# Kernel tuning notes

Measured on AMD Instinct MI355X. Metric: run time of the kernel, lower is better.

Reference implementation:

```python
import jax, jax.numpy as jnp
import numpy as np

ATT = 16          # attention_size -> window = 2*ATT+1 = 33
HID = 512         # middle hidden size


def setup_inputs() -> dict:
    key = jax.random.key(0)
    ks = jax.random.split(key, 7)
    B, S, D_IN = 4, 2048, 256
    def xav(k, shape):
        fan_in, fan_out = shape[0], shape[1]
        std = np.sqrt(2.0 / (fan_in + fan_out))
        return jax.random.normal(k, shape, dtype=jnp.float32) * std
    return {
        "x": jax.random.normal(ks[0], (B, S, D_IN), dtype=jnp.float32),
        "Wq": xav(ks[1], (HID, HID)),
        "Wk": xav(ks[2], (HID, HID)),
        "Wv": xav(ks[3], (HID, HID)),
        "W0": xav(ks[4], (D_IN, HID)),
        "b0": jnp.zeros((1, 1, HID), dtype=jnp.float32),
        "W1": xav(ks[5], (HID, HID)),
        "b1": jnp.zeros((1, 1, HID), dtype=jnp.float32),
        "Wout": xav(ks[6], (HID, 2)),
        "bout": jnp.zeros((1, 1, 2), dtype=jnp.float32),
    }


def _local_windows(h, A):
    # h: [B, S, H] -> nei: [B, S, 2A+1, H], nei[b,t,j] = h[b, t+A-j] (zero padded)
    S = h.shape[1]
    padded = jnp.pad(h, ((0, 0), (A, A), (0, 0)))
    t = jnp.arange(S)[:, None]
    j = jnp.arange(2 * A + 1)[None, :]
    idx = t + 2 * A - j  # padded index of h[t + A - j]
    return padded[:, idx, :]


def reference(x, Wq, Wk, Wv, W0, b0, W1, b1, Wout, bout):
    scale = jnp.float32(np.sqrt(float(HID)))
    # pre-attention MLP layer(s)
    h = jax.nn.relu(x @ W0 + b0)                       # [B,S,H]
    nei = _local_windows(h, ATT)                       # [B,S,W,H]
    q = h @ Wq                                         # [B,S,H]
    k = nei @ Wk                                       # [B,S,W,H]
    v = nei @ Wv                                       # [B,S,W,H]
    dist = jnp.einsum('bsd,bswd->bsw', q, k) / scale   # [B,S,W]
    attn = jax.nn.softmax(dist, axis=-1)               # [B,S,W]
    ctx = jnp.einsum('bsw,bswd->bsd', attn, v)         # [B,S,H]
    # post-attention MLP layers
    h2 = jax.nn.relu(ctx @ W1 + b1)
    out = h2 @ Wout + bout                             # [B,S,2]
    return out, attn[:, :, None, :]  # attn shape [B,S,1,W] as in torch
```

## Files before the change

kernel.cpp:

```cpp
#include <hip/hip_runtime.h>

#define S_LEN 2048
#define HID 512
#define DIN 256
#define WIN 33
#define MROWS 8192
#define VTB 2080
#define VTROW 8320
#define SCALE_INV 0.04419417382415922f

typedef __attribute__((ext_vector_type(8))) short short8;
typedef __attribute__((ext_vector_type(4))) float f32x4;

__device__ __forceinline__ unsigned short f2bf(float f) {
    unsigned u = __builtin_bit_cast(unsigned, f);
    u += 0x7fffu + ((u >> 16) & 1u);
    return (unsigned short)(u >> 16);
}
__device__ __forceinline__ float bf2f(unsigned short h) {
    unsigned u = ((unsigned)h) << 16;
    return __builtin_bit_cast(float, u);
}
__device__ __forceinline__ void gl_lds16(const unsigned short* g, unsigned short* l) {
    __builtin_amdgcn_global_load_lds(
        (__attribute__((address_space(1))) unsigned int*)(g),
        (__attribute__((address_space(3))) unsigned int*)(l),
        16, 0, 0);
}

__global__ __launch_bounds__(256) void prep_kernel(
    const float* __restrict__ x,
    const float* __restrict__ Wq, const float* __restrict__ Wk,
    const float* __restrict__ Wv, const float* __restrict__ W0,
    const float* __restrict__ W1, const float* __restrict__ bout,
    unsigned short* __restrict__ xb, unsigned short* __restrict__ Wt0,
    unsigned short* __restrict__ Wtqkv, unsigned short* __restrict__ Wt1,
    unsigned short* __restrict__ Vt, float* __restrict__ outp)
{
    __shared__ float tile[32][33];
    const int blk = blockIdx.x, tid = threadIdx.x;
    if (blk < 2048) {
        int i = (blk * 256 + tid) * 4;
        float4 v = *(const float4*)(x + i);
        unsigned lo = (unsigned)f2bf(v.x) | ((unsigned)f2bf(v.y) << 16);
        unsigned hi = (unsigned)f2bf(v.z) | ((unsigned)f2bf(v.w) << 16);
        uint2 p; p.x = lo; p.y = hi;
        *(uint2*)(xb + i) = p;
    } else if (blk < 2064) {
        int i = ((blk - 2048) * 256 + tid) * 4;
        float4 o; o.x = bout[0]; o.y = bout[1]; o.z = bout[0]; o.w = bout[1];
        *(float4*)(outp + i) = o;
    } else if (blk < 2320) {
        int t = (blk - 2064) * 256 + tid;
        int v = t >> 7, s = t & 127;
        int b = s >> 5, p = s & 31;
        int off = (p < 16) ? p : (2048 + p);
        Vt[(size_t)v * VTROW + b * VTB + off] = 0;
    } else {
        int tt = blk - 2320;
        const float* in; unsigned short* out; int K, kt, nt;
        if (tt < 128) { in = W0; out = Wt0; K = DIN; kt = tt & 7; nt = tt >> 3; }
        else {
            int z = (tt - 128) >> 8, r = (tt - 128) & 255;
            kt = r & 15; nt = r >> 4; K = HID;
            if (z == 0)      { in = Wq; out = Wtqkv; }
            else if (z == 1) { in = Wk; out = Wtqkv + 512 * 512; }
            else if (z == 2) { in = Wv; out = Wtqkv + 2 * 512 * 512; }
            else             { in = W1; out = Wt1; }
        }
        int k0 = kt * 32, n0 = nt * 32;
        int tx = tid & 31, ty = tid >> 5;
        for (int j = 0; j < 32; j += 8)
            tile[ty + j][tx] = in[(size_t)(k0 + ty + j) * HID + n0 + tx];
        __syncthreads();
        for (int j = 0; j < 32; j += 8)
            out[(size_t)(n0 + ty + j) * K + k0 + tx] = f2bf(tile[tx][ty + j]);
    }
}

template<int K, int MODE>
__global__ __launch_bounds__(256) void gemm128_kernel(
    const unsigned short* __restrict__ A,
    const unsigned short* __restrict__ Bt,
    const float* __restrict__ bias,
    unsigned short* __restrict__ C0,
    unsigned short* __restrict__ C1,
    unsigned short* __restrict__ C2,
    const float* __restrict__ Wout,
    float* __restrict__ outp)
{
    __shared__ __align__(16) unsigned short SMEM[16384];
    const int tid = threadIdx.x;
    const int lane = tid & 63, wid = tid >> 6;
    const int bn = blockIdx.x, bm = blockIdx.y;
    const int wr = wid >> 1, wc = wid & 1;
    const int r16 = lane & 15, kq = lane >> 4;
    const int NT = K / 32;

    f32x4 acc[4][4] = {};

    const int c0 = tid, c1 = tid + 256;
    const unsigned short* aS0 = A + (size_t)(bm * 128 + (c0 & 127)) * K + (c0 >> 7) * 8;
    const unsigned short* aS1 = A + (size_t)(bm * 128 + (c1 & 127)) * K + (c1 >> 7) * 8;
    const unsigned short* bS0 = Bt + (size_t)(bn * 128 + (c0 & 127)) * K + (c0 >> 7) * 8;
    const unsigned short* bS1 = Bt + (size_t)(bn * 128 + (c1 & 127)) * K + (c1 >> 7) * 8;

    #define STAGE(buf, kt) do { \
        gl_lds16(aS0 + (kt) * 32, SMEM + (buf) * 8192 + c0 * 8); \
        gl_lds16(aS1 + (kt) * 32, SMEM + (buf) * 8192 + c1 * 8); \
        gl_lds16(bS0 + (kt) * 32, SMEM + (buf) * 8192 + 4096 + c0 * 8); \
        gl_lds16(bS1 + (kt) * 32, SMEM + (buf) * 8192 + 4096 + c1 * 8); \
    } while (0)

    STAGE(0, 0);
    for (int kt = 0; kt < NT; ++kt) {
        const int cur = kt & 1;
        if (kt + 1 < NT) {
            STAGE(cur ^ 1, kt + 1);
            asm volatile("s_waitcnt vmcnt(4)" ::: "memory");
        } else {
            asm volatile("s_waitcnt vmcnt(0)" ::: "memory");
        }
        __builtin_amdgcn_sched_barrier(0);
        __builtin_amdgcn_s_barrier();
        __builtin_amdgcn_sched_barrier(0);

        const unsigned short* ab = SMEM + cur * 8192;
        const unsigned short* bb = ab + 4096;
        short8 af[4], bfr[4];
        #pragma unroll
        for (int mi = 0; mi < 4; ++mi)
            af[mi] = *(const short8*)(ab + kq * 1024 + (wr * 64 + mi * 16 + r16) * 8);
        #pragma unroll
        for (int ni = 0; ni < 4; ++ni)
            bfr[ni] = *(const short8*)(bb + kq * 1024 + (wc * 64 + ni * 16 + r16) * 8);
        #pragma unroll
        for (int mi = 0; mi < 4; ++mi)
            #pragma unroll
            for (int ni = 0; ni < 4; ++ni)
                acc[mi][ni] = __builtin_amdgcn_mfma_f32_16x16x32_bf16(af[mi], bfr[ni], acc[mi][ni], 0, 0, 0);

        asm volatile("s_waitcnt lgkmcnt(0)" ::: "memory");
        __builtin_amdgcn_sched_barrier(0);
        __builtin_amdgcn_s_barrier();
        __builtin_amdgcn_sched_barrier(0);
    }
    #undef STAGE

    if constexpr (MODE == 0) {
        #pragma unroll
        for (int mi = 0; mi < 4; ++mi) {
            int row0 = bm * 128 + wr * 64 + mi * 16 + kq * 4;
            #pragma unroll
            for (int ni = 0; ni < 4; ++ni) {
                int col = bn * 128 + wc * 64 + ni * 16 + r16;
                float bv = bias[col];
                #pragma unroll
                for (int r = 0; r < 4; ++r) {
                    float v = fmaxf(acc[mi][ni][r] + bv, 0.0f);
                    C0[(size_t)(row0 + r) * HID + col] = f2bf(v);
                }
            }
        }
    } else if constexpr (MODE == 1) {
        if (bn < 8) {
            unsigned short* dst = (bn < 4) ? C0 : C1;
            int cb = (bn & 3) * 128 + wc * 64;
            #pragma unroll
            for (int mi = 0; mi < 4; ++mi) {
                int row0 = bm * 128 + wr * 64 + mi * 16 + kq * 4;
                #pragma unroll
                for (int ni = 0; ni < 4; ++ni) {
                    int col = cb + ni * 16 + r16;
                    #pragma unroll
                    for (int r = 0; r < 4; ++r)
                        dst[(size_t)(row0 + r) * HID + col] = f2bf(acc[mi][ni][r]);
                }
            }
        } else {
            const int bb  = (bm * 128) >> 11;
            const int tl0 = (bm * 128) & 2047;
            #pragma unroll
            for (int p = 0; p < 2; ++p) {
                if (wc == p) {
                    #pragma unroll
                    for (int mi = 0; mi < 4; ++mi) {
                        int ttw = wr * 64 + mi * 16 + kq * 4;
                        #pragma unroll
                        for (int ni = 0; ni < 4; ++ni) {
                            int vv = ni * 16 + r16;
                            unsigned lo = (unsigned)f2bf(acc[mi][ni][0]) | ((unsigned)f2bf(acc[mi][ni][1]) << 16);
                            unsigned hi = (unsigned)f2bf(acc[mi][ni][2]) | ((unsigned)f2bf(acc[mi][ni][3]) << 16);
                            uint2 pk; pk.x = lo; pk.y = hi;
                            *(uint2*)&SMEM[vv * 128 + (ttw ^ ((vv & 7) << 3))] = pk;
                        }
                    }
                }
                __syncthreads();
                #pragma unroll
                for (int it = 0; it < 4; ++it) {
                    int vv  = (tid >> 4) + it * 16;
                    int tt8 = (tid & 15) * 8;
                    uint4 q = *(const uint4*)&SMEM[vv * 128 + (tt8 ^ ((vv & 7) << 3))];
                    int vg = (bn - 8) * 128 + p * 64 + vv;
                    *(uint4*)(C2 + (size_t)vg * VTROW + bb * VTB + 16 + tl0 + tt8) = q;
                }
                __syncthreads();
            }
        }
    } else {
        float o0[16], o1[16];
        #pragma unroll
        for (int t2 = 0; t2 < 16; ++t2) { o0[t2] = 0.0f; o1[t2] = 0.0f; }
        #pragma unroll
        for (int ni = 0; ni < 4; ++ni) {
            int col = bn * 128 + wc * 64 + ni * 16 + r16;
            float bv = bias[col];
            float2 wv = *(const float2*)(Wout + col * 2);
            #pragma unroll
            for (int mi = 0; mi < 4; ++mi)
                #pragma unroll
                for (int r = 0; r < 4; ++r) {
                    float v = fmaxf(acc[mi][ni][r] + bv, 0.0f);
                    o0[mi * 4 + r] += v * wv.x;
                    o1[mi * 4 + r] += v * wv.y;
                }
        }
        #pragma unroll
        for (int s = 1; s < 16; s <<= 1)
            #pragma unroll
            for (int t2 = 0; t2 < 16; ++t2) {
                o0[t2] += __shfl_xor(o0[t2], s);
                o1[t2] += __shfl_xor(o1[t2], s);
            }
        if (r16 == 0) {
            #pragma unroll
            for (int mi = 0; mi < 4; ++mi)
                #pragma unroll
                for (int r = 0; r < 4; ++r) {
                    int row = bm * 128 + wr * 64 + mi * 16 + kq * 4 + r;
                    atomicAdd(&outp[(size_t)row * 2],     o0[mi * 4 + r]);
                    atomicAdd(&outp[(size_t)row * 2 + 1], o1[mi * 4 + r]);
                }
        }
    }
}

__global__ __launch_bounds__(256) void attn_kernel(
    const unsigned short* __restrict__ Qb,
    const unsigned short* __restrict__ Kb,
    const unsigned short* __restrict__ Vt,
    float* __restrict__ attn_out,
    unsigned short* __restrict__ ctx)
{
    __shared__ __align__(16) float Sl[4][32][66];
    __shared__ __align__(16) unsigned short Pl[32 * 64];
    const int tid = threadIdx.x;
    const int lane = tid & 63;
    const int w = tid >> 6;
    const int t0g = blockIdx.x * 32;
    const int b = t0g >> 11;
    const int t0 = t0g & 2047;
    const int r16 = lane & 15, kq = lane >> 4;

    f32x4 s[2][4] = {};
    const unsigned short* qbase = Qb + (size_t)t0g * HID + w * 128 + kq * 8;
    const unsigned short* kbase = Kb + (long)(t0g - 16) * HID + w * 128 + kq * 8;
    #pragma unroll
    for (int ks = 0; ks < 4; ++ks) {
        short8 a0 = *(const short8*)(qbase + (size_t)r16 * HID + ks * 32);
        short8 a1 = *(const short8*)(qbase + (size_t)(16 + r16) * HID + ks * 32);
        #pragma unroll
        for (int ni = 0; ni < 4; ++ni) {
            short8 bf = *(const short8*)(kbase + (size_t)(ni * 16 + r16) * HID + ks * 32);
            s[0][ni] = __builtin_amdgcn_mfma_f32_16x16x32_bf16(a0, bf, s[0][ni], 0, 0, 0);
            s[1][ni] = __builtin_amdgcn_mfma_f32_16x16x32_bf16(a1, bf, s[1][ni], 0, 0, 0);
        }
    }
    #pragma unroll
    for (int mi = 0; mi < 2; ++mi)
        #pragma unroll
        for (int ni = 0; ni < 4; ++ni)
            #pragma unroll
            for (int r = 0; r < 4; ++r)
                Sl[w][mi * 16 + kq * 4 + r][ni * 16 + r16] = s[mi][ni][r];
    __syncthreads();

    {
        const int i = tid >> 3;
        const int c8 = (tid & 7) * 8;
        float sv[8];
        #pragma unroll
        for (int cc = 0; cc < 8; ++cc) {
            float a = Sl[0][i][c8 + cc] + Sl[1][i][c8 + cc]
                    + Sl[2][i][c8 + cc] + Sl[3][i][c8 + cc];
            int m = c8 + cc;
            bool inb = (m >= i) && (m <= i + 32);
            int krow = t0 + m - 16;
            bool inseq = (krow >= 0) && (krow < S_LEN);
            sv[cc] = inb ? (inseq ? a * SCALE_INV : 0.0f) : -INFINITY;
        }
        float mx = sv[0];
        #pragma unroll
        for (int cc = 1; cc < 8; ++cc) mx = fmaxf(mx, sv[cc]);
        mx = fmaxf(mx, __shfl_xor(mx, 1));
        mx = fmaxf(mx, __shfl_xor(mx, 2));
        mx = fmaxf(mx, __shfl_xor(mx, 4));
        float es = 0.0f;
        #pragma unroll
        for (int cc = 0; cc < 8; ++cc) { sv[cc] = __expf(sv[cc] - mx); es += sv[cc]; }
        es += __shfl_xor(es, 1);
        es += __shfl_xor(es, 2);
        es += __shfl_xor(es, 4);
        float inv = 1.0f / es;
        unsigned short pb[8];
        #pragma unroll
        for (int cc = 0; cc < 8; ++cc) {
            float p = sv[cc] * inv;
            pb[cc] = f2bf(p);
            int m = c8 + cc;
            if (m >= i && m <= i + 32)
                attn_out[(size_t)(t0g + i) * WIN + (i + 32 - m)] = p;
        }
        uint4 pk;
        pk.x = (unsigned)pb[0] | ((unsigned)pb[1] << 16);
        pk.y = (unsigned)pb[2] | ((unsigned)pb[3] << 16);
        pk.z = (unsigned)pb[4] | ((unsigned)pb[5] << 16);
        pk.w = (unsigned)pb[6] | ((unsigned)pb[7] << 16);
        *(uint4*)((char*)Pl + i * 128 + ((c8 * 2) ^ ((i & 7) << 4))) = pk;
    }
    __syncthreads();

    f32x4 c[2][8] = {};
    const char* plb = (const char*)Pl;
    const unsigned short* vtb = Vt + (size_t)b * VTB + t0;
    #pragma unroll
    for (int ks = 0; ks < 2; ++ks) {
        int cb = ks * 64 + kq * 16;
        short8 a0 = *(const short8*)(plb + r16 * 128 + (cb ^ ((r16 & 7) << 4)));
        short8 a1 = *(const short8*)(plb + (16 + r16) * 128 + (cb ^ ((r16 & 7) << 4)));
        #pragma unroll
        for (int nd = 0; nd < 8; ++nd) {
            const unsigned short* vp = vtb + (size_t)(w * 128 + nd * 16 + r16) * VTROW + ks * 32 + kq * 8;
            short8 bf = *(const short8*)vp;
            c[0][nd] = __builtin_amdgcn_mfma_f32_16x16x32_bf16(a0, bf, c[0][nd], 0, 0, 0);
            c[1][nd] = __builtin_amdgcn_mfma_f32_16x16x32_bf16(a1, bf, c[1][nd], 0, 0, 0);
        }
    }
    #pragma unroll
    for (int mi = 0; mi < 2; ++mi) {
        int row0 = t0g + mi * 16 + kq * 4;
        #pragma unroll
        for (int nd = 0; nd < 8; ++nd) {
            int col = w * 128 + nd * 16 + r16;
            #pragma unroll
            for (int r = 0; r < 4; ++r)
                ctx[(size_t)(row0 + r) * HID + col] = f2bf(c[mi][nd][r]);
        }
    }
}

extern "C" void kernel_launch(void* const* d_in, const int* in_sizes, int n_in,
                              void* d_out, int out_size, void* d_ws, size_t ws_size,
                              hipStream_t stream)
{
    const float* x    = (const float*)d_in[0];
    const float* Wq   = (const float*)d_in[1];
    const float* Wk   = (const float*)d_in[2];
    const float* Wv   = (const float*)d_in[3];
    const float* W0   = (const float*)d_in[4];
    const float* b0   = (const float*)d_in[5];
    const float* W1   = (const float*)d_in[6];
    const float* b1   = (const float*)d_in[7];
    const float* Wout = (const float*)d_in[8];
    const float* bout = (const float*)d_in[9];

    char* ws = (char*)d_ws;
    unsigned short* xb    = (unsigned short*)(ws + 0);
    unsigned short* Wt0   = (unsigned short*)(ws + (4u  << 20));
    unsigned short* Wtqkv = (unsigned short*)(ws + 4456448u);
    unsigned short* Wt1   = (unsigned short*)(ws + 6029312u);
    unsigned short* hB    = (unsigned short*)(ws + (8u  << 20));
    unsigned short* Qb    = (unsigned short*)(ws + (16u << 20));
    unsigned short* Kb    = (unsigned short*)(ws + (24u << 20));
    unsigned short* Vt    = (unsigned short*)(ws + (32u << 20));
    unsigned short* ctxB  = (unsigned short*)(ws + (41u << 20));

    float* outp  = (float*)d_out;
    float* attnp = (float*)d_out + MROWS * 2;

    prep_kernel<<<3472, 256, 0, stream>>>(x, Wq, Wk, Wv, W0, W1, bout,
                                          xb, Wt0, Wtqkv, Wt1, Vt, outp);

    gemm128_kernel<DIN, 0><<<dim3(4, 64), 256, 0, stream>>>(
        xb, Wt0, b0, hB, nullptr, nullptr, nullptr, nullptr);

    gemm128_kernel<HID, 1><<<dim3(12, 64), 256, 0, stream>>>(
        hB, Wtqkv, nullptr, Qb, Kb, Vt, nullptr, nullptr);

    attn_kernel<<<256, 256, 0, stream>>>(Qb, Kb, Vt, attnp, ctxB);

    gemm128_kernel<HID, 2><<<dim3(4, 64), 256, 0, stream>>>(
        ctxB, Wt1, b1, nullptr, nullptr, nullptr, Wout, outp);
}
```

Baseline: 147.8 us.

## Fuse post-attention MLP and output projection into the attention kernel

The attention kernel now keeps the context tile in LDS and runs the ctx@W1 GEMM, ReLU and Wout projection itself, writing final outputs directly with bout added. This removes the separate GEMM launch, the ctx round-trip through global memory, and the atomicAdd reduction. In exchange each of only 256 blocks does a 32x512x512 GEMM reading W1 from global/L2 without LDS staging, which may lower parallelism and raise LDS use per block.

New measurement: 151.1 us. +2.2%, slower.

```diff
diff --git a/kernel.cpp b/kernel.cpp
--- a/kernel.cpp
+++ b/kernel.cpp
@@ -85,9 +85,7 @@
     const float* __restrict__ bias,
     unsigned short* __restrict__ C0,
     unsigned short* __restrict__ C1,
-    unsigned short* __restrict__ C2,
-    const float* __restrict__ Wout,
-    float* __restrict__ outp)
+    unsigned short* __restrict__ C2)
 {
     __shared__ __align__(16) unsigned short SMEM[16384];
     const int tid = threadIdx.x;
@@ -162,7 +160,7 @@
                 }
             }
         }
-    } else if constexpr (MODE == 1) {
+    } else {
         if (bn < 8) {
             unsigned short* dst = (bn < 4) ? C0 : C1;
             int cb = (bn & 3) * 128 + wc * 64;
@@ -208,41 +206,6 @@
                 __syncthreads();
             }
         }
-    } else {
-        float o0[16], o1[16];
-        #pragma unroll
-        for (int t2 = 0; t2 < 16; ++t2) { o0[t2] = 0.0f; o1[t2] = 0.0f; }
-        #pragma unroll
-        for (int ni = 0; ni < 4; ++ni) {
-            int col = bn * 128 + wc * 64 + ni * 16 + r16;
-            float bv = bias[col];
-            float2 wv = *(const float2*)(Wout + col * 2);
-            #pragma unroll
-            for (int mi = 0; mi < 4; ++mi)
-                #pragma unroll
-                for (int r = 0; r < 4; ++r) {
-                    float v = fmaxf(acc[mi][ni][r] + bv, 0.0f);
-                    o0[mi * 4 + r] += v * wv.x;
-                    o1[mi * 4 + r] += v * wv.y;
-                }
-        }
-        #pragma unroll
-        for (int s = 1; s < 16; s <<= 1)
-            #pragma unroll
-            for (int t2 = 0; t2 < 16; ++t2) {
-                o0[t2] += __shfl_xor(o0[t2], s);
-                o1[t2] += __shfl_xor(o1[t2], s);
-            }
-        if (r16 == 0) {
-            #pragma unroll
-            for (int mi = 0; mi < 4; ++mi)
-                #pragma unroll
-                for (int r = 0; r < 4; ++r) {
-                    int row = bm * 128 + wr * 64 + mi * 16 + kq * 4 + r;
-                    atomicAdd(&outp[(size_t)row * 2],     o0[mi * 4 + r]);
-                    atomicAdd(&outp[(size_t)row * 2 + 1], o1[mi * 4 + r]);
-                }
-        }
     }
 }
 
@@ -250,11 +213,17 @@
     const unsigned short* __restrict__ Qb,
     const unsigned short* __restrict__ Kb,
     const unsigned short* __restrict__ Vt,
+    const unsigned short* __restrict__ W1t,
+    const float* __restrict__ b1,
+    const float* __restrict__ Wout,
+    const float* __restrict__ bout,
     float* __restrict__ attn_out,
-    unsigned short* __restrict__ ctx)
+    float* __restrict__ outp)
 {
     __shared__ __align__(16) float Sl[4][32][66];
     __shared__ __align__(16) unsigned short Pl[32 * 64];
+    __shared__ __align__(16) unsigned short Cl[32 * 512];
+    __shared__ float Ol[4][32][2];
     const int tid = threadIdx.x;
     const int lane = tid & 63;
     const int w = tid >> 6;
@@ -332,31 +301,95 @@
     __syncthreads();
 
     f32x4 c[2][8] = {};
-    const char* plb = (const char*)Pl;
-    const unsigned short* vtb = Vt + (size_t)b * VTB + t0;
+    {
+        const char* plb = (const char*)Pl;
+        const unsigned short* vtb = Vt + (size_t)b * VTB + t0;
+        #pragma unroll
+        for (int ks = 0; ks < 2; ++ks) {
+            int cb = ks * 64 + kq * 16;
+            short8 a0 = *(const short8*)(plb + r16 * 128 + (cb ^ ((r16 & 7) << 4)));
+            short8 a1 = *(const short8*)(plb + (16 + r16) * 128 + (cb ^ ((r16 & 7) << 4)));
+            #pragma unroll
+            for (int nd = 0; nd < 8; ++nd) {
+                const unsigned short* vp = vtb + (size_t)(w * 128 + nd * 16 + r16) * VTROW + ks * 32 + kq * 8;
+                short8 bf = *(const short8*)vp;
+                c[0][nd] = __builtin_amdgcn_mfma_f32_16x16x32_bf16(a0, bf, c[0][nd], 0, 0, 0);
+                c[1][nd] = __builtin_amdgcn_mfma_f32_16x16x32_bf16(a1, bf, c[1][nd], 0, 0, 0);
+            }
+        }
+    }
+
     #pragma unroll
-    for (int ks = 0; ks < 2; ++ks) {
-        int cb = ks * 64 + kq * 16;
-        short8 a0 = *(const short8*)(plb + r16 * 128 + (cb ^ ((r16 & 7) << 4)));
-        short8 a1 = *(const short8*)(plb + (16 + r16) * 128 + (cb ^ ((r16 & 7) << 4)));
-        #pragma unroll
-        for (int nd = 0; nd < 8; ++nd) {
-            const unsigned short* vp = vtb + (size_t)(w * 128 + nd * 16 + r16) * VTROW + ks * 32 + kq * 8;
-            short8 bf = *(const short8*)vp;
-            c[0][nd] = __builtin_amdgcn_mfma_f32_16x16x32_bf16(a0, bf, c[0][nd], 0, 0, 0);
-            c[1][nd] = __builtin_amdgcn_mfma_f32_16x16x32_bf16(a1, bf, c[1][nd], 0, 0, 0);
-        }
-    }
-    #pragma unroll
-    for (int mi = 0; mi < 2; ++mi) {
-        int row0 = t0g + mi * 16 + kq * 4;
-        #pragma unroll
-        for (int nd = 0; nd < 8; ++nd) {
-            int col = w * 128 + nd * 16 + r16;
-            #pragma unroll
-            for (int r = 0; r < 4; ++r)
-                ctx[(size_t)(row0 + r) * HID + col] = f2bf(c[mi][nd][r]);
-        }
+    for (int mi = 0; mi < 2; ++mi)
+        #pragma unroll
+        for (int nd = 0; nd < 8; ++nd)
+            #pragma unroll
+            for (int r = 0; r < 4; ++r) {
+                int row = mi * 16 + kq * 4 + r;
+                int byte = row * 1024 + (w * 128 + nd * 16 + r16) * 2;
+                *(unsigned short*)((char*)Cl + (byte ^ ((row & 7) << 4))) = f2bf(c[mi][nd][r]);
+            }
+    __syncthreads();
+
+    f32x4 g[2][8] = {};
+    {
+        const char* clb = (const char*)Cl;
+        const unsigned short* w1b = W1t + (size_t)(w * 128) * HID + kq * 8;
+        #pragma unroll 4
+        for (int ks = 0; ks < 16; ++ks) {
+            int r0 = r16, r1 = 16 + r16;
+            short8 af0 = *(const short8*)(clb + ((r0 * 1024 + ks * 64 + kq * 16) ^ ((r0 & 7) << 4)));
+            short8 af1 = *(const short8*)(clb + ((r1 * 1024 + ks * 64 + kq * 16) ^ ((r1 & 7) << 4)));
+            #pragma unroll
+            for (int ni = 0; ni < 8; ++ni) {
+                short8 bf = *(const short8*)(w1b + (size_t)(ni * 16 + r16) * HID + ks * 32);
+                g[0][ni] = __builtin_amdgcn_mfma_f32_16x16x32_bf16(af0, bf, g[0][ni], 0, 0, 0);
+                g[1][ni] = __builtin_amdgcn_mfma_f32_16x16x32_bf16(af1, bf, g[1][ni], 0, 0, 0);
+            }
+        }
+    }
+
+    {
+        float o0[8], o1[8];
+        #pragma unroll
+        for (int t2 = 0; t2 < 8; ++t2) { o0[t2] = 0.0f; o1[t2] = 0.0f; }
+        #pragma unroll
+        for (int ni = 0; ni < 8; ++ni) {
+            int col = w * 128 + ni * 16 + r16;
+            float bv = b1[col];
+            float2 wv = *(const float2*)(Wout + col * 2);
+            #pragma unroll
+            for (int mi = 0; mi < 2; ++mi)
+                #pragma unroll
+                for (int r = 0; r < 4; ++r) {
+                    float v = fmaxf(g[mi][ni][r] + bv, 0.0f);
+                    o0[mi * 4 + r] += v * wv.x;
+                    o1[mi * 4 + r] += v * wv.y;
+                }
+        }
+        #pragma unroll
+        for (int s2 = 1; s2 < 16; s2 <<= 1)
+            #pragma unroll
+            for (int t2 = 0; t2 < 8; ++t2) {
+                o0[t2] += __shfl_xor(o0[t2], s2);
+                o1[t2] += __shfl_xor(o1[t2], s2);
+            }
+        if (r16 == 0) {
+            #pragma unroll
+            for (int mi = 0; mi < 2; ++mi)
+                #pragma unroll
+                for (int r = 0; r < 4; ++r) {
+                    int row = mi * 16 + kq * 4 + r;
+                    Ol[w][row][0] = o0[mi * 4 + r];
+                    Ol[w][row][1] = o1[mi * 4 + r];
+                }
+        }
+    }
+    __syncthreads();
+    if (tid < 64) {
+        int row = tid >> 1, cc = tid & 1;
+        float sum = Ol[0][row][cc] + Ol[1][row][cc] + Ol[2][row][cc] + Ol[3][row][cc] + bout[cc];
+        outp[(size_t)(t0g + row) * 2 + cc] = sum;
     }
 }
 
@@ -384,7 +417,6 @@
     unsigned short* Qb    = (unsigned short*)(ws + (16u << 20));
     unsigned short* Kb    = (unsigned short*)(ws + (24u << 20));
     unsigned short* Vt    = (unsigned short*)(ws + (32u << 20));
-    unsigned short* ctxB  = (unsigned short*)(ws + (41u << 20));
 
     float* outp  = (float*)d_out;
     float* attnp = (float*)d_out + MROWS * 2;
@@ -393,13 +425,11 @@
                                           xb, Wt0, Wtqkv, Wt1, Vt, outp);
 
     gemm128_kernel<DIN, 0><<<dim3(4, 64), 256, 0, stream>>>(
-        xb, Wt0, b0, hB, nullptr, nullptr, nullptr, nullptr);
+        xb, Wt0, b0, hB, nullptr, nullptr);
 
     gemm128_kernel<HID, 1><<<dim3(12, 64), 256, 0, stream>>>(
-        hB, Wtqkv, nullptr, Qb, Kb, Vt, nullptr, nullptr);
-
-    attn_kernel<<<256, 256, 0, stream>>>(Qb, Kb, Vt, attnp, ctxB);
-
-    gemm128_kernel<HID, 2><<<dim3(4, 64), 256, 0, stream>>>(
-        ctxB, Wt1, b1, nullptr, nullptr, nullptr, Wout, outp);
-}
+        hB, Wtqkv, nullptr, Qb, Kb, Vt);
+
+    attn_kernel<<<256, 256, 0, stream>>>(Qb, Kb, Vt, Wt1, b1, Wout, bout,
+                                         attnp, outp);
+}
```
